# Kernel tuning notes

Measured on AMD Instinct MI355X. Metric: run time of the kernel, lower is better.

## Reference

```python
import jax, jax.numpy as jnp
import numpy as np

B = 262144
HID = 256
HEADS = 8


def setup_inputs() -> dict:
    key = jax.random.key(0)
    ks = jax.random.split(key, 8)
    s = 1.0 / np.sqrt(HID)
    return {
        "fine_messages": jax.random.normal(ks[0], (B, HID), jnp.float32),
        "coarse_messages": jax.random.normal(ks[1], (B, HID), jnp.float32),
        "motif_features": jax.random.normal(ks[2], (B, HID), jnp.float32),
        "Wq": jax.random.normal(ks[3], (HID, HID), jnp.float32) * s,
        "Wk": jax.random.normal(ks[4], (HID, HID), jnp.float32) * s,
        "Wv": jax.random.normal(ks[5], (HID, HID), jnp.float32) * s,
        "Wo": jax.random.normal(ks[6], (HID, HID), jnp.float32) * s,
        "bo": jax.random.normal(ks[7], (HID,), jnp.float32) * s,
        "heads": HEADS,
    }


def reference(fine_messages, coarse_messages, motif_features, Wq, Wk, Wv, Wo, bo, heads):
    b, hid = motif_features.shape
    d_k = hid // heads
    # K/V share the same pre-projection input: [fine; coarse] -> (B, 2, hid)
    kv_in = jnp.stack([fine_messages, coarse_messages], axis=1)
    # torch Linear(x) = x @ W.T (no bias on q/k/v projections)
    q = (motif_features @ Wq.T).reshape(b, heads, d_k)          # (B, H, d_k) single query
    k = (kv_in @ Wk.T).reshape(b, 2, heads, d_k)                # (B, 2, H, d_k)
    v = (kv_in @ Wv.T).reshape(b, 2, heads, d_k)
    # NOTE: original divides by d_k, not sqrt(d_k)
    scores = jnp.einsum("bhd,bshd->bhs", q, k) / d_k            # (B, H, 2)
    att = jax.nn.softmax(scores, axis=-1)
    out = jnp.einsum("bhs,bshd->bhd", att, v).reshape(b, hid)   # (B, hid)
    return out @ Wo.T + bo
```

## Files before the change

kernel.cpp:

```cpp
#include <hip/hip_runtime.h>

#define B_TOT 262144
#define HID   256
#define NHEAD 8
#define BR    64
#define NTHR  256

typedef __bf16 bf16_t;
typedef __attribute__((ext_vector_type(8))) __bf16 bf16x8;
typedef __attribute__((ext_vector_type(4))) float  f32x4;

#define WPK_BYTES (512 * 1024)

#define PHASE_SYNC(N)                                                  \
  do {                                                                 \
    asm volatile("s_waitcnt vmcnt(" #N ") lgkmcnt(0)" ::: "memory");   \
    __builtin_amdgcn_s_barrier();                                      \
  } while (0)

static __device__ __forceinline__ f32x4 mfma16(bf16x8 a, bf16x8 b, f32x4 c) {
  return __builtin_amdgcn_mfma_f32_16x16x32_bf16(a, b, c, 0, 0, 0);
}

static __device__ __forceinline__ bf16x8 cvt8(float4 a, float4 b) {
  bf16x8 r;
  r[0] = (bf16_t)a.x; r[1] = (bf16_t)a.y; r[2] = (bf16_t)a.z; r[3] = (bf16_t)a.w;
  r[4] = (bf16_t)b.x; r[5] = (bf16_t)b.y; r[6] = (bf16_t)b.z; r[7] = (bf16_t)b.w;
  return r;
}

static __device__ __forceinline__ bf16x8 pin8(bf16x8 v) {
  f32x4 t = __builtin_bit_cast(f32x4, v);
  asm volatile("" : "+v"(t));
  return __builtin_bit_cast(bf16x8, t);
}

typedef __attribute__((address_space(3))) void lds_void;
typedef __attribute__((address_space(1))) void gbl_void;
static __device__ __forceinline__ void gload_lds16(const void* g, void* l) {
  __builtin_amdgcn_global_load_lds((gbl_void*)g, (lds_void*)l, 16, 0, 0);
}

__global__ __launch_bounds__(256) void pack_weights(
    const float* __restrict__ Wq, const float* __restrict__ Wk,
    const float* __restrict__ Wv, const float* __restrict__ Wo,
    bf16_t* __restrict__ ws) {
  const int t     = blockIdx.x * 256 + threadIdx.x;
  const int lane  = t & 63;
  const int chunk = t >> 6;
  const int l15 = lane & 15, lg = lane >> 4;
  const float* src;
  int row, col;
  if (chunk < 384) {
    const int ph = chunk >> 4;
    const int c  = chunk & 15;
    const int h = ph / 3, w = ph % 3;
    const int ks = c >> 1, half = c & 1;
    src = (w == 0) ? Wq : (w == 1) ? Wk : Wv;
    row = h * 32 + (l15 >> 2) * 8 + half * 4 + (l15 & 3);
    col = ks * 32 + lg * 8;
  } else {
    const int c  = chunk - 384;
    const int ks = c >> 4, jt = c & 15;
    src = Wo;
    row = jt * 16 + l15;
    col = ks * 32 + lg * 8;
  }
  const float* p = src + (size_t)row * HID + col;
  *(bf16x8*)(ws + (size_t)t * 8) = cvt8(*(const float4*)p, *(const float4*)(p + 4));
}

__global__ __launch_bounds__(NTHR, 3) void fused_local_aug(
    const float* __restrict__ fine, const float* __restrict__ coarse,
    const float* __restrict__ motif, const bf16_t* __restrict__ wpk,
    bf16_t* __restrict__ mid, const float* __restrict__ bo,
    float* __restrict__ out) {
  __shared__ char wbuf[49152];

  const int tid  = threadIdx.x;
  const int lane = tid & 63;
  const int wave = tid >> 6;
  const int l15  = lane & 15;
  const int lg   = lane >> 4;
  const size_t mrow = (size_t)blockIdx.x * BR + wave * 16 + l15;
  bf16_t* midp = mid + mrow * HID + lg * 8;

  auto stage = [&](int ph) {
    char* dst = wbuf + (ph % 3) * 16384 + tid * 16;
    const char* src = (const char*)wpk + (size_t)ph * 16384 + tid * 16;
#pragma unroll
    for (int i = 0; i < 4; ++i)
      gload_lds16(src + i * 4096, dst + i * 4096);
  };

  stage(0);
  stage(1);

  bf16x8 xm[8], xf[8], xc[8];
  {
    const float* pm = motif  + mrow * HID + lg * 8;
    const float* pf = fine   + mrow * HID + lg * 8;
    const float* pc = coarse + mrow * HID + lg * 8;
#pragma unroll
    for (int s = 0; s < 8; ++s) {
      xm[s] = pin8(cvt8(*(const float4*)(pm + s * 32), *(const float4*)(pm + s * 32 + 4)));
      xf[s] = pin8(cvt8(*(const float4*)(pf + s * 32), *(const float4*)(pf + s * 32 + 4)));
      xc[s] = pin8(cvt8(*(const float4*)(pc + s * 32), *(const float4*)(pc + s * 32 + 4)));
    }
  }
  __syncthreads();

  const f32x4 z4 = {0.f, 0.f, 0.f, 0.f};

  f32x4 aQ0, aQ1, aK10, aK11, aK20, aK21, aV10, aV11, aV20, aV21;
  float ps1, ps2;
  bf16x8 mf7;

  auto finish_head = [&](int h) {
    float s1 = ps1, s2 = ps2;
    s1 += __shfl_xor(s1, 16); s1 += __shfl_xor(s1, 32);
    s2 += __shfl_xor(s2, 16); s2 += __shfl_xor(s2, 32);
    s1 *= (1.0f / 32.0f);  s2 *= (1.0f / 32.0f);
    const float mx = fmaxf(s1, s2);
    const float e1 = __expf(s1 - mx), e2 = __expf(s2 - mx);
    const float a1 = e1 / (e1 + e2);
    const float a2 = 1.0f - a1;
    bf16x8 t;
#pragma unroll
    for (int r = 0; r < 4; ++r) {
      t[r]     = (bf16_t)(a1 * aV10[r] + a2 * aV20[r]);
      t[r + 4] = (bf16_t)(a1 * aV11[r] + a2 * aV21[r]);
    }
    if (h < NHEAD - 1) *(bf16x8*)(midp + h * 32) = t;
    else               mf7 = t;
  };

#pragma unroll
  for (int h = 0; h < NHEAD; ++h) {
    {
      const int p = 3 * h;
      if (p > 0) PHASE_SYNC(4);
      stage(p + 2);
      aQ0 = z4; aQ1 = z4;
      const char* pb = wbuf + (p % 3) * 16384 + lane * 16;
      __builtin_amdgcn_s_setprio(1);
#pragma unroll
      for (int ks = 0; ks < 8; ++ks) {
        bf16x8 q0 = *(const bf16x8*)(pb + ks * 2048);
        bf16x8 q1 = *(const bf16x8*)(pb + ks * 2048 + 1024);
        aQ0 = mfma16(q0, xm[ks], aQ0);
        aQ1 = mfma16(q1, xm[ks], aQ1);
      }
      __builtin_amdgcn_s_setprio(0);
      if (h > 0) finish_head(h - 1);
    }
    {
      const int p = 3 * h + 1;
      PHASE_SYNC(4);
      stage(p + 2);
      aK10 = z4; aK11 = z4; aK20 = z4; aK21 = z4;
      const char* pb = wbuf + (p % 3) * 16384 + lane * 16;
      __builtin_amdgcn_s_setprio(1);
#pragma unroll
      for (int ks = 0; ks < 8; ++ks) {
        bf16x8 k0 = *(const bf16x8*)(pb + ks * 2048);
        bf16x8 k1 = *(const bf16x8*)(pb + ks * 2048 + 1024);
        aK10 = mfma16(k0, xf[ks], aK10);
        aK11 = mfma16(k1, xf[ks], aK11);
        aK20 = mfma16(k0, xc[ks], aK20);
        aK21 = mfma16(k1, xc[ks], aK21);
      }
      __builtin_amdgcn_s_setprio(0);
    }
    {
      const int p = 3 * h + 2;
      PHASE_SYNC(4);
      stage(p + 2);
      aV10 = z4; aV11 = z4; aV20 = z4; aV21 = z4;
      const char* pb = wbuf + (p % 3) * 16384 + lane * 16;
      __builtin_amdgcn_s_setprio(1);
#pragma unroll
      for (int ks = 0; ks < 8; ++ks) {
        bf16x8 v0 = *(const bf16x8*)(pb + ks * 2048);
        bf16x8 v1 = *(const bf16x8*)(pb + ks * 2048 + 1024);
        aV10 = mfma16(v0, xf[ks], aV10);
        aV11 = mfma16(v1, xf[ks], aV11);
        aV20 = mfma16(v0, xc[ks], aV20);
        aV21 = mfma16(v1, xc[ks], aV21);
      }
      __builtin_amdgcn_s_setprio(0);
      float s1 = 0.f, s2 = 0.f;
#pragma unroll
      for (int r = 0; r < 4; ++r) {
        s1 += aQ0[r] * aK10[r] + aQ1[r] * aK11[r];
        s2 += aQ0[r] * aK20[r] + aQ1[r] * aK21[r];
      }
      ps1 = s1; ps2 = s2;
    }
  }
  finish_head(NHEAD - 1);

  bf16x8 mf[NHEAD];
#pragma unroll
  for (int s = 0; s < 7; ++s) mf[s] = *(const bf16x8*)(midp + s * 32);
  mf[7] = mf7;

  f32x4 acc[16];
#pragma unroll
  for (int jt = 0; jt < 16; ++jt) acc[jt] = z4;

#pragma unroll
  for (int wp = 0; wp < 8; ++wp) {
    const int p = 24 + wp;
    if (wp == 7) { PHASE_SYNC(0); } else { PHASE_SYNC(4); }
    if (wp < 6) stage(p + 2);
    bf16x8 m = mf[wp];
    const char* pb = wbuf + (p % 3) * 16384 + lane * 16;
    __builtin_amdgcn_s_setprio(1);
#pragma unroll
    for (int jt = 0; jt < 16; ++jt) {
      bf16x8 wf = *(const bf16x8*)(pb + jt * 1024);
      acc[jt] = mfma16(wf, m, acc[jt]);
    }
    __builtin_amdgcn_s_setprio(0);
  }

#pragma unroll
  for (int jt = 0; jt < 16; ++jt) {
    const int jj = jt * 16 + lg * 4;
    const float4 b4 = *(const float4*)(bo + jj);
    f32x4 o;
    o[0] = acc[jt][0] + b4.x;
    o[1] = acc[jt][1] + b4.y;
    o[2] = acc[jt][2] + b4.z;
    o[3] = acc[jt][3] + b4.w;
    __builtin_nontemporal_store(o, (f32x4*)(out + mrow * HID + jj));
  }
}

extern "C" void kernel_launch(void* const* d_in, const int* in_sizes, int n_in,
                              void* d_out, int out_size, void* d_ws, size_t ws_size,
                              hipStream_t stream) {
  (void)in_sizes; (void)n_in; (void)ws_size; (void)out_size;
  const float* fine   = (const float*)d_in[0];
  const float* coarse = (const float*)d_in[1];
  const float* motif  = (const float*)d_in[2];
  const float* Wq     = (const float*)d_in[3];
  const float* Wk     = (const float*)d_in[4];
  const float* Wv     = (const float*)d_in[5];
  const float* Wo     = (const float*)d_in[6];
  const float* bo     = (const float*)d_in[7];
  float* out          = (float*)d_out;
  bf16_t* wpk         = (bf16_t*)d_ws;
  bf16_t* mid         = (bf16_t*)((char*)d_ws + WPK_BYTES);

  pack_weights<<<128, 256, 0, stream>>>(Wq, Wk, Wv, Wo, wpk);
  fused_local_aug<<<B_TOT / BR, NTHR, 0, stream>>>(fine, coarse, motif, wpk,
                                                   mid, bo, out);
}
```

Baseline: 388.9 us.

## Deepen weight staging to 4 LDS buffers, register-prefetch half of next phase, drop mid scratch

Switches weight staging from a 3-buffer to a 4-buffer LDS ring, so each phase is staged three ahead. At the end of each phase it also copies the first half of the next phase's weight fragments into registers. The per-head attention outputs now stay in registers instead of round-tripping through a global bf16 scratch buffer, and the score reduction moves earlier into the K phase. The aim is to hide LDS and global latency behind MFMA work, at the cost of 64KB LDS and more registers, which lowers the occupancy target from 3 to 2 blocks per CU.

Measured after the change: 341.6 us. 1.14x faster.

```diff
diff --git a/kernel.cpp b/kernel.cpp
--- a/kernel.cpp
+++ b/kernel.cpp
@@ -10,7 +10,6 @@
 typedef __attribute__((ext_vector_type(8))) __bf16 bf16x8;
 typedef __attribute__((ext_vector_type(4))) float  f32x4;
 
-#define WPK_BYTES (512 * 1024)
 
 #define PHASE_SYNC(N)                                                  \
   do {                                                                 \
@@ -70,12 +69,11 @@
   *(bf16x8*)(ws + (size_t)t * 8) = cvt8(*(const float4*)p, *(const float4*)(p + 4));
 }
 
-__global__ __launch_bounds__(NTHR, 3) void fused_local_aug(
+__global__ __launch_bounds__(NTHR, 2) void fused_local_aug(
     const float* __restrict__ fine, const float* __restrict__ coarse,
     const float* __restrict__ motif, const bf16_t* __restrict__ wpk,
-    bf16_t* __restrict__ mid, const float* __restrict__ bo,
-    float* __restrict__ out) {
-  __shared__ char wbuf[49152];
+    const float* __restrict__ bo, float* __restrict__ out) {
+  __shared__ char wbuf[65536];
 
   const int tid  = threadIdx.x;
   const int lane = tid & 63;
@@ -83,10 +81,9 @@
   const int l15  = lane & 15;
   const int lg   = lane >> 4;
   const size_t mrow = (size_t)blockIdx.x * BR + wave * 16 + l15;
-  bf16_t* midp = mid + mrow * HID + lg * 8;
 
   auto stage = [&](int ph) {
-    char* dst = wbuf + (ph % 3) * 16384 + tid * 16;
+    char* dst = wbuf + (ph & 3) * 16384 + tid * 16;
     const char* src = (const char*)wpk + (size_t)ph * 16384 + tid * 16;
 #pragma unroll
     for (int i = 0; i < 4; ++i)
@@ -95,6 +92,7 @@
 
   stage(0);
   stage(1);
+  stage(2);
 
   bf16x8 xm[8], xf[8], xc[8];
   {
@@ -110,13 +108,20 @@
   }
   __syncthreads();
 
+  bf16x8 wpre[2][8];
+  {
+    const char* pb = wbuf + lane * 16;
+#pragma unroll
+    for (int c = 0; c < 8; ++c) wpre[0][c] = *(const bf16x8*)(pb + c * 1024);
+  }
+
+  bf16x8 mfrag[NHEAD];
   const f32x4 z4 = {0.f, 0.f, 0.f, 0.f};
 
   f32x4 aQ0, aQ1, aK10, aK11, aK20, aK21, aV10, aV11, aV20, aV21;
-  float ps1, ps2;
-  bf16x8 mf7;
-
-  auto finish_head = [&](int h) {
+  float ps1 = 0.f, ps2 = 0.f;
+
+  auto finish = [&](int hh) {
     float s1 = ps1, s2 = ps2;
     s1 += __shfl_xor(s1, 16); s1 += __shfl_xor(s1, 32);
     s2 += __shfl_xor(s2, 16); s2 += __shfl_xor(s2, 32);
@@ -131,8 +136,14 @@
       t[r]     = (bf16_t)(a1 * aV10[r] + a2 * aV20[r]);
       t[r + 4] = (bf16_t)(a1 * aV11[r] + a2 * aV21[r]);
     }
-    if (h < NHEAD - 1) *(bf16x8*)(midp + h * 32) = t;
-    else               mf7 = t;
+    mfrag[hh] = t;
+  };
+
+  auto prefetch_next = [&](int p) {
+    const char* pn = wbuf + ((p + 1) & 3) * 16384 + lane * 16;
+#pragma unroll
+    for (int c = 0; c < 8; ++c)
+      wpre[(p + 1) & 1][c] = *(const bf16x8*)(pn + c * 1024);
   };
 
 #pragma unroll
@@ -140,29 +151,44 @@
     {
       const int p = 3 * h;
       if (p > 0) PHASE_SYNC(4);
-      stage(p + 2);
+      stage(p + 3);
       aQ0 = z4; aQ1 = z4;
-      const char* pb = wbuf + (p % 3) * 16384 + lane * 16;
+      const char* pb = wbuf + (p & 3) * 16384 + lane * 16;
       __builtin_amdgcn_s_setprio(1);
 #pragma unroll
-      for (int ks = 0; ks < 8; ++ks) {
+      for (int ks = 0; ks < 4; ++ks) {
+        aQ0 = mfma16(wpre[p & 1][ks * 2],     xm[ks], aQ0);
+        aQ1 = mfma16(wpre[p & 1][ks * 2 + 1], xm[ks], aQ1);
+      }
+#pragma unroll
+      for (int ks = 4; ks < 8; ++ks) {
         bf16x8 q0 = *(const bf16x8*)(pb + ks * 2048);
         bf16x8 q1 = *(const bf16x8*)(pb + ks * 2048 + 1024);
         aQ0 = mfma16(q0, xm[ks], aQ0);
         aQ1 = mfma16(q1, xm[ks], aQ1);
       }
       __builtin_amdgcn_s_setprio(0);
-      if (h > 0) finish_head(h - 1);
+      prefetch_next(p);
+      if (h > 0) finish(h - 1);
     }
     {
       const int p = 3 * h + 1;
       PHASE_SYNC(4);
-      stage(p + 2);
+      stage(p + 3);
       aK10 = z4; aK11 = z4; aK20 = z4; aK21 = z4;
-      const char* pb = wbuf + (p % 3) * 16384 + lane * 16;
+      const char* pb = wbuf + (p & 3) * 16384 + lane * 16;
       __builtin_amdgcn_s_setprio(1);
 #pragma unroll
-      for (int ks = 0; ks < 8; ++ks) {
+      for (int ks = 0; ks < 4; ++ks) {
+        bf16x8 k0 = wpre[p & 1][ks * 2];
+        bf16x8 k1 = wpre[p & 1][ks * 2 + 1];
+        aK10 = mfma16(k0, xf[ks], aK10);
+        aK11 = mfma16(k1, xf[ks], aK11);
+        aK20 = mfma16(k0, xc[ks], aK20);
+        aK21 = mfma16(k1, xc[ks], aK21);
+      }
+#pragma unroll
+      for (int ks = 4; ks < 8; ++ks) {
         bf16x8 k0 = *(const bf16x8*)(pb + ks * 2048);
         bf16x8 k1 = *(const bf16x8*)(pb + ks * 2048 + 1024);
         aK10 = mfma16(k0, xf[ks], aK10);
@@ -171,16 +197,35 @@
         aK21 = mfma16(k1, xc[ks], aK21);
       }
       __builtin_amdgcn_s_setprio(0);
+      prefetch_next(p);
+      {
+        float s1 = 0.f, s2 = 0.f;
+#pragma unroll
+        for (int r = 0; r < 4; ++r) {
+          s1 += aQ0[r] * aK10[r] + aQ1[r] * aK11[r];
+          s2 += aQ0[r] * aK20[r] + aQ1[r] * aK21[r];
+        }
+        ps1 = s1; ps2 = s2;
+      }
     }
     {
       const int p = 3 * h + 2;
       PHASE_SYNC(4);
-      stage(p + 2);
+      stage(p + 3);
       aV10 = z4; aV11 = z4; aV20 = z4; aV21 = z4;
-      const char* pb = wbuf + (p % 3) * 16384 + lane * 16;
+      const char* pb = wbuf + (p & 3) * 16384 + lane * 16;
       __builtin_amdgcn_s_setprio(1);
 #pragma unroll
-      for (int ks = 0; ks < 8; ++ks) {
+      for (int ks = 0; ks < 4; ++ks) {
+        bf16x8 v0 = wpre[p & 1][ks * 2];
+        bf16x8 v1 = wpre[p & 1][ks * 2 + 1];
+        aV10 = mfma16(v0, xf[ks], aV10);
+        aV11 = mfma16(v1, xf[ks], aV11);
+        aV20 = mfma16(v0, xc[ks], aV20);
+        aV21 = mfma16(v1, xc[ks], aV21);
+      }
+#pragma unroll
+      for (int ks = 4; ks < 8; ++ks) {
         bf16x8 v0 = *(const bf16x8*)(pb + ks * 2048);
         bf16x8 v1 = *(const bf16x8*)(pb + ks * 2048 + 1024);
         aV10 = mfma16(v0, xf[ks], aV10);
@@ -189,21 +234,10 @@
         aV21 = mfma16(v1, xc[ks], aV21);
       }
       __builtin_amdgcn_s_setprio(0);
-      float s1 = 0.f, s2 = 0.f;
-#pragma unroll
-      for (int r = 0; r < 4; ++r) {
-        s1 += aQ0[r] * aK10[r] + aQ1[r] * aK11[r];
-        s2 += aQ0[r] * aK20[r] + aQ1[r] * aK21[r];
-      }
-      ps1 = s1; ps2 = s2;
-    }
-  }
-  finish_head(NHEAD - 1);
-
-  bf16x8 mf[NHEAD];
-#pragma unroll
-  for (int s = 0; s < 7; ++s) mf[s] = *(const bf16x8*)(midp + s * 32);
-  mf[7] = mf7;
+      prefetch_next(p);
+    }
+  }
+  finish(NHEAD - 1);
 
   f32x4 acc[16];
 #pragma unroll
@@ -212,17 +246,21 @@
 #pragma unroll
   for (int wp = 0; wp < 8; ++wp) {
     const int p = 24 + wp;
-    if (wp == 7) { PHASE_SYNC(0); } else { PHASE_SYNC(4); }
-    if (wp < 6) stage(p + 2);
-    bf16x8 m = mf[wp];
-    const char* pb = wbuf + (p % 3) * 16384 + lane * 16;
+    if (wp <= 5) { PHASE_SYNC(4); } else { PHASE_SYNC(0); }
+    if (wp <= 4) stage(p + 3);
+    bf16x8 m = mfrag[wp];
+    const char* pb = wbuf + (p & 3) * 16384 + lane * 16;
     __builtin_amdgcn_s_setprio(1);
 #pragma unroll
-    for (int jt = 0; jt < 16; ++jt) {
+    for (int jt = 0; jt < 8; ++jt)
+      acc[jt] = mfma16(wpre[p & 1][jt], m, acc[jt]);
+#pragma unroll
+    for (int jt = 8; jt < 16; ++jt) {
       bf16x8 wf = *(const bf16x8*)(pb + jt * 1024);
       acc[jt] = mfma16(wf, m, acc[jt]);
     }
     __builtin_amdgcn_s_setprio(0);
+    if (wp < 7) prefetch_next(p);
   }
 
 #pragma unroll
@@ -252,9 +290,7 @@
   const float* bo     = (const float*)d_in[7];
   float* out          = (float*)d_out;
   bf16_t* wpk         = (bf16_t*)d_ws;
-  bf16_t* mid         = (bf16_t*)((char*)d_ws + WPK_BYTES);
 
   pack_weights<<<128, 256, 0, stream>>>(Wq, Wk, Wv, Wo, wpk);
-  fused_local_aug<<<B_TOT / BR, NTHR, 0, stream>>>(fine, coarse, motif, wpk,
-                                                   mid, bo, out);
-}
+  fused_local_aug<<<B_TOT / BR, NTHR, 0, stream>>>(fine, coarse, motif, wpk, bo, out);
+}
```
